# Performance work log

Measured on AMD Instinct MI355X. Metric: run time of the kernel, lower is better.

## Reference

```python
import jax, jax.numpy as jnp
import numpy as np

SQRT_QKV_DIM = 8.0  # sqrt(qkv_dim=64)


def setup_inputs() -> dict:
    key = jax.random.key(0)
    ks = jax.random.split(key, 8)
    B, H, T, M, d, hid = 4, 16, 512, 512, 64, 16
    return {
        "q": jax.random.normal(ks[0], (B, H, T, d), dtype=jnp.float32),
        "k": jax.random.normal(ks[1], (B, H, M, d), dtype=jnp.float32),
        "v": jax.random.normal(ks[2], (B, H, M, d), dtype=jnp.float32),
        "D_TM": jax.random.uniform(ks[3], (B, T, M), dtype=jnp.float32),
        "mix1_weight": jax.random.uniform(ks[4], (H, 2, hid), minval=-0.7071, maxval=0.7071, dtype=jnp.float32),
        "mix1_bias": jax.random.uniform(ks[5], (H, hid), minval=-0.7071, maxval=0.7071, dtype=jnp.float32),
        "mix2_weight": jax.random.uniform(ks[6], (H, hid, 1), minval=-0.25, maxval=0.25, dtype=jnp.float32),
        "mix2_bias": jax.random.uniform(ks[7], (H, 1), minval=-0.25, maxval=0.25, dtype=jnp.float32),
    }


def reference(q, k, v, D_TM, mix1_weight, mix1_bias, mix2_weight, mix2_bias):
    B, H, T, d = q.shape
    Mc = k.shape[2]
    # scaled dot-product score: (B,H,T,M)
    dot_score = jnp.einsum("bhtd,bhmd->bhtm", q, k) / SQRT_QKV_DIM
    # per-head 2->hidden->1 MLP mixing dot score and distance bias.
    # Avoid explicit stack: linear layer over the 2 score channels expands as
    # dot*W1[:,0,:] + D*W1[:,1,:].  ms1: (B,H,T,M,hid)
    w1_dot = mix1_weight[:, 0, :][None, :, None, None, :]   # (1,H,1,1,hid)
    w1_dist = mix1_weight[:, 1, :][None, :, None, None, :]
    ms1 = (dot_score[..., None] * w1_dot
           + D_TM[:, None, :, :, None] * w1_dist
           + mix1_bias[None, :, None, None, :])
    ms1 = jax.nn.relu(ms1)
    # hidden -> 1: mixed_scores (B,H,T,M)
    mixed = jnp.einsum("bhtmc,hc->bhtm", ms1, mix2_weight[:, :, 0])
    mixed = mixed + mix2_bias[:, 0][None, :, None, None]
    weights = jax.nn.softmax(mixed, axis=3)
    out = jnp.einsum("bhtm,bhmd->bhtd", weights, v)   # (B,H,T,d)
    return out.transpose(0, 2, 1, 3).reshape(B, T, H * d)
```

## Files before the change

### kernel.cpp

```cpp
#include <hip/hip_runtime.h>
#include <stdint.h>

typedef __attribute__((ext_vector_type(8))) short short8;
typedef __attribute__((ext_vector_type(4))) float floatx4;

#define MFMA(a, b, c) __builtin_amdgcn_mfma_f32_16x16x32_bf16(a, b, c, 0, 0, 0)

union Frag { uint32_t u[4]; short8 s; };

__device__ __forceinline__ void packsplit(float a, float b, uint32_t& hi, uint32_t& lo) {
    uint32_t ua = __float_as_uint(a), ub = __float_as_uint(b);
    uint32_t ha = ua & 0xFFFF0000u, hb = ub & 0xFFFF0000u;
    float ra = a - __uint_as_float(ha);
    float rb = b - __uint_as_float(hb);
    hi = __builtin_amdgcn_perm(ub, ua, 0x07060302u);
    lo = __builtin_amdgcn_perm(__float_as_uint(rb), __float_as_uint(ra), 0x07060302u);
}

__device__ __forceinline__ float fexp2(float x) {
#if __has_builtin(__builtin_amdgcn_exp2f)
    return __builtin_amdgcn_exp2f(x);
#else
    return exp2f(x);
#endif
}

__device__ __forceinline__ void bar_lds() {
    asm volatile("s_waitcnt lgkmcnt(0)" ::: "memory");
    __builtin_amdgcn_s_barrier();
    __builtin_amdgcn_sched_barrier(0);
}


__attribute__((amdgpu_waves_per_eu(4)))
__global__ __launch_bounds__(512)
void msmha_flash(const float* __restrict__ qg, const float* __restrict__ kg,
                 const float* __restrict__ vg, const float* __restrict__ Dg,
                 const float* __restrict__ m1w, const float* __restrict__ m1b,
                 const float* __restrict__ m2w, const float* __restrict__ m2b,
                 float* __restrict__ outg) {
    __shared__ __align__(16) uint32_t sm[17408];
    __shared__ __align__(16) float4 wlds[16];

    const int tid   = threadIdx.x;
    const int w     = tid >> 6;
    const int group = w >> 2;
    const int gw    = w & 3;
    const int lane  = tid & 63;
    const int col   = lane & 15;
    const int quad  = lane >> 4;
    const int gtid  = tid & 255;

    const int bid = blockIdx.x;
    const int wgT = bid >> 6;
    const int bh  = bid & 63;
    const int h   = bh & 15;
    const int b   = bh >> 4;
    const int t0g = wgT * 64;

    const size_t base = (size_t)bh * 512 * 64;
    const float LOG2E = 1.4426950408889634f;

    if (tid < 16) {
        const float w1d = m1w[h * 32 + tid];
        const float w1s = m1w[h * 32 + 16 + tid];
        const float b1  = m1b[h * 16 + tid];
        const float w2  = m2w[h * 16 + tid];
        wlds[tid] = make_float4(w1d * (0.125f * LOG2E), w1s * LOG2E, b1 * LOG2E, 0.5f * w2);
    }

    const int krow = 16 * gw + (lane >> 2);
    const int kqt  = lane & 3;
    const int ksw  = (krow & 7) << 2;
    const int rsw  = (col & 7) << 2;
    const int dgrp = gtid & 15;
    const int m4   = gtid >> 4;
    const int cpV  = (2 * m4 + 8 * ((dgrp >> 1) & 3)) & 31;
    const int rsel = col >> 3;

    const int gb = group * 8704;
    uint32_t* KH = sm + gb;
    uint32_t* KL = sm + gb + 2048;
    uint32_t* VH = sm + gb + 4096;
    uint32_t* VL = sm + gb + 6400;

    const int moff = group * 256;
    const float* kc = kg + base + (size_t)moff * 64;
    const float* vc = vg + base + (size_t)moff * 64;
    const float* Dc = Dg + ((size_t)b * 512 + t0g + gw * 16 + col) * 512 + moff + quad * 4;

    float sA = 0.f, sB = 0.f, sC = 0.f;
#pragma unroll 1
    for (int c = 0; c < 16; ++c) {
        const float w2 = m2w[h * 16 + c];
        sA = fmaf(w2, m1w[h * 32 + c], sA);
        sB = fmaf(w2, m1w[h * 32 + 16 + c], sB);
        sC = fmaf(w2, m1b[h * 16 + c], sC);
    }
    const float Ac = sA * (0.0625f * LOG2E);
    const float Bc = sB * (0.5f * LOG2E);
    const float Cc = fmaf(0.5f, sC, m2b[h]) * LOG2E;

    Frag qh[2], ql[2];
    {
        const float* qrow = qg + base + (size_t)(t0g + gw * 16 + col) * 64;
#pragma unroll
        for (int ks = 0; ks < 2; ++ks) {
            const float4 f0 = *(const float4*)(qrow + ks * 32 + quad * 8);
            const float4 f1 = *(const float4*)(qrow + ks * 32 + quad * 8 + 4);
            packsplit(f0.x, f0.y, qh[ks].u[0], ql[ks].u[0]);
            packsplit(f0.z, f0.w, qh[ks].u[1], ql[ks].u[1]);
            packsplit(f1.x, f1.y, qh[ks].u[2], ql[ks].u[2]);
            packsplit(f1.z, f1.w, qh[ks].u[3], ql[ks].u[3]);
        }
    }

    float lsum = 0.f;
    floatx4 oacc[4];
#pragma unroll
    for (int dt = 0; dt < 4; ++dt) oacc[dt] = floatx4{0.f, 0.f, 0.f, 0.f};

#pragma unroll 1
    for (int mc = 0; mc < 4; ++mc) {
        float4 kp[4], vp[4], dp[4];
#pragma unroll
        for (int i = 0; i < 4; ++i)
            kp[i] = *(const float4*)(kc + (size_t)(mc * 64 + krow) * 64 + 16 * i + 4 * kqt);
#pragma unroll
        for (int i = 0; i < 4; ++i)
            vp[i] = *(const float4*)(vc + (size_t)(mc * 64 + 4 * m4 + i) * 64 + dgrp * 4);
#pragma unroll
        for (int mt = 0; mt < 4; ++mt)
            dp[mt] = *(const float4*)(Dc + mc * 64 + mt * 16);

#pragma unroll
        for (int i = 0; i < 4; ++i) {
            uint32_t h0, l0, h1, l1;
            packsplit(kp[i].x, kp[i].y, h0, l0);
            packsplit(kp[i].z, kp[i].w, h1, l1);
            const int off = (8 * i + 2 * kqt) ^ ksw;
            *(uint2*)(KH + krow * 32 + off) = make_uint2(h0, h1);
            *(uint2*)(KL + krow * 32 + off) = make_uint2(l0, l1);
        }
        bar_lds();

        floatx4 sc[4];
        __builtin_amdgcn_s_setprio(1);
#pragma unroll
        for (int mt = 0; mt < 4; ++mt) {
            floatx4 acc = {0.f, 0.f, 0.f, 0.f};
#pragma unroll
            for (int ks = 0; ks < 2; ++ks) {
                const int ro = (mt * 16 + col) * 32 + ((16 * ks + 4 * quad) ^ rsw);
                Frag ah, al;
                ah.s = *(const short8*)(KH + ro);
                al.s = *(const short8*)(KL + ro);
                acc = MFMA(ah.s, qh[ks].s, acc);
                acc = MFMA(ah.s, ql[ks].s, acc);
                acc = MFMA(al.s, qh[ks].s, acc);
            }
            sc[mt] = acc;
        }
        __builtin_amdgcn_s_setprio(0);

#pragma unroll
        for (int jj = 0; jj < 4; ++jj) {
            uint32_t h0, l0, h1, l1;
            packsplit(((const float*)&vp[0])[jj], ((const float*)&vp[1])[jj], h0, l0);
            packsplit(((const float*)&vp[2])[jj], ((const float*)&vp[3])[jj], h1, l1);
            const int d = 4 * dgrp + jj;
            *(uint2*)(VH + d * 36 + cpV) = make_uint2(h0, h1);
            *(uint2*)(VL + d * 36 + cpV) = make_uint2(l0, l1);
        }

#pragma unroll
        for (int half = 0; half < 2; ++half) {
            float dvf[8], mix[8];
#pragma unroll
            for (int q2 = 0; q2 < 2; ++q2) {
                const float4 dd = dp[2 * half + q2];
                dvf[q2 * 4 + 0] = dd.x; dvf[q2 * 4 + 1] = dd.y;
                dvf[q2 * 4 + 2] = dd.z; dvf[q2 * 4 + 3] = dd.w;
            }
#pragma unroll
            for (int e = 0; e < 8; ++e) mix[e] = fmaf(dvf[e], Bc, Cc);
#pragma unroll 4
            for (int c = 0; c < 16; ++c) {
                const float4 wv = wlds[c];
#pragma unroll
                for (int e = 0; e < 8; ++e) {
                    const float s = sc[2 * half + (e >> 2)][e & 3];
                    const float hh = fmaf(s, wv.x, fmaf(dvf[e], wv.y, wv.z));
                    mix[e] = fmaf(fabsf(hh), wv.w, mix[e]);
                }
            }
#pragma unroll
            for (int e = 0; e < 8; ++e) {
                const float s = sc[2 * half + (e >> 2)][e & 3];
                const float p = fexp2(fmaf(s, Ac, mix[e]));
                sc[2 * half + (e >> 2)][e & 3] = p;
                lsum += p;
            }
        }

        bar_lds();

        const int prow = (gw * 16 + col) * 32;
#pragma unroll
        for (int mt = 0; mt < 4; ++mt) {
            uint32_t h0, l0, h1, l1;
            packsplit(sc[mt][0], sc[mt][1], h0, l0);
            packsplit(sc[mt][2], sc[mt][3], h1, l1);
            const int off = (mt * 8 + 2 * quad) ^ rsw;
            *(uint2*)(KH + prow + off) = make_uint2(h0, h1);
            *(uint2*)(KL + prow + off) = make_uint2(l0, l1);
        }

        __builtin_amdgcn_s_setprio(1);
#pragma unroll
        for (int ks = 0; ks < 2; ++ks) {
            const int po = prow + ((16 * ks + 4 * quad) ^ rsw);
            Frag pah, pal;
            pah.s = *(const short8*)(KH + po);
            pal.s = *(const short8*)(KL + po);
#pragma unroll
            for (int dt = 0; dt < 4; ++dt) {
                const int cbd = ((16 * ks + 4 * quad) + 8 * ((2 * dt + rsel) & 3)) & 31;
                const int vo = (dt * 16 + col) * 36 + cbd;
                Frag bhv, blv;
                bhv.s = *(const short8*)(VH + vo);
                blv.s = *(const short8*)(VL + vo);
                oacc[dt] = MFMA(pah.s, bhv.s, oacc[dt]);
                oacc[dt] = MFMA(pah.s, blv.s, oacc[dt]);
                oacc[dt] = MFMA(pal.s, bhv.s, oacc[dt]);
            }
        }
        __builtin_amdgcn_s_setprio(0);
    }

    bar_lds();

    lsum += __shfl_xor(lsum, 16, 64);
    lsum += __shfl_xor(lsum, 32, 64);

    float* smf = (float*)sm;
    if (group == 1) {
        if (quad == 0) smf[12864 + gw * 16 + col] = lsum;
        const int t = gw * 16 + quad * 4;
#pragma unroll
        for (int dt = 0; dt < 4; ++dt)
#pragma unroll
            for (int r = 0; r < 4; ++r)
                smf[8704 + (t + r) * 65 + dt * 16 + col] = oacc[dt][r];
    }
    bar_lds();
    if (group == 0) {
        const float l1c = smf[12864 + gw * 16 + col];
        const float rdn = 1.f / (lsum + l1c);
        float rdT[4];
#pragma unroll
        for (int r = 0; r < 4; ++r)
            rdT[r] = __shfl(rdn, quad * 4 + r, 64);
        const int t = gw * 16 + quad * 4;
        const size_t obase = ((size_t)b * 512 + t0g + t) * 1024 + h * 64 + col;
#pragma unroll
        for (int dt = 0; dt < 4; ++dt)
#pragma unroll
            for (int r = 0; r < 4; ++r) {
                const float o1 = smf[8704 + (t + r) * 65 + dt * 16 + col];
                outg[obase + (size_t)r * 1024 + dt * 16] = (oacc[dt][r] + o1) * rdT[r];
            }
    }
}

extern "C" void kernel_launch(void* const* d_in, const int* in_sizes, int n_in,
                              void* d_out, int out_size, void* d_ws, size_t ws_size,
                              hipStream_t stream) {
    const float* q   = (const float*)d_in[0];
    const float* k   = (const float*)d_in[1];
    const float* v   = (const float*)d_in[2];
    const float* dtm = (const float*)d_in[3];
    const float* m1w = (const float*)d_in[4];
    const float* m1b = (const float*)d_in[5];
    const float* m2w = (const float*)d_in[6];
    const float* m2b = (const float*)d_in[7];
    float* out = (float*)d_out;

    dim3 grid(4 * 16 * 8);
    dim3 block(512);
    msmha_flash<<<grid, block, 0, stream>>>(q, k, v, dtm, m1w, m1b, m2w, m2b, out);
}
```

Measured before the change: 123.9 us.

## Pre-pack K/V into bf16 hi/lo split once and vectorize MLP mixing with packed float2

```diff
diff --git a/kernel.cpp b/kernel.cpp
--- a/kernel.cpp
+++ b/kernel.cpp
@@ -3,10 +3,12 @@
 
 typedef __attribute__((ext_vector_type(8))) short short8;
 typedef __attribute__((ext_vector_type(4))) float floatx4;
+typedef __attribute__((ext_vector_type(2))) float float2v;
 
 #define MFMA(a, b, c) __builtin_amdgcn_mfma_f32_16x16x32_bf16(a, b, c, 0, 0, 0)
 
 union Frag { uint32_t u[4]; short8 s; };
+union PF2 { float2v f; uint32_t u[2]; };
 
 __device__ __forceinline__ void packsplit(float a, float b, uint32_t& hi, uint32_t& lo) {
     uint32_t ua = __float_as_uint(a), ub = __float_as_uint(b);
@@ -31,13 +33,53 @@
     __builtin_amdgcn_sched_barrier(0);
 }
 
-
-__attribute__((amdgpu_waves_per_eu(4)))
-__global__ __launch_bounds__(512)
+#define VLO 1048576
+#define KPK_DW 2097152
+#define WS_NEED ((size_t)(KPK_DW + 2 * VLO) * 4)
+
+__global__ __launch_bounds__(256)
+void packkv(const float* __restrict__ kg, const float* __restrict__ vg,
+            uint32_t* __restrict__ kpk, uint32_t* __restrict__ vpk) {
+    const int bid = blockIdx.x, tid = threadIdx.x;
+    if (bid < 2048) {
+        const int g   = bid * 256 + tid;
+        const int row = g >> 4, q = g & 15;
+        const float4 f = *(const float4*)(kg + (size_t)row * 64 + 4 * q);
+        uint32_t h0, l0, h1, l1;
+        packsplit(f.x, f.y, h0, l0);
+        packsplit(f.z, f.w, h1, l1);
+        uint32_t* rb = kpk + (size_t)row * 64;
+        *(uint2*)(rb + 2 * q)      = make_uint2(h0, h1);
+        *(uint2*)(rb + 32 + 2 * q) = make_uint2(l0, l1);
+    } else {
+        const int vb  = bid - 2048;
+        const int bh  = vb >> 4, m2g = vb & 15;
+        const int m2  = m2g * 16 + (tid & 15);
+        const int dg  = tid >> 4;
+        const float* r0 = vg + ((size_t)(bh * 512 + 2 * m2)) * 64 + 4 * dg;
+        const float4 f0 = *(const float4*)(r0);
+        const float4 f1 = *(const float4*)(r0 + 64);
+        const float a0[4] = {f0.x, f0.y, f0.z, f0.w};
+        const float a1[4] = {f1.x, f1.y, f1.z, f1.w};
+#pragma unroll
+        for (int jj = 0; jj < 4; ++jj) {
+            uint32_t hh, ll;
+            packsplit(a0[jj], a1[jj], hh, ll);
+            const size_t o = (size_t)(bh * 64 + 4 * dg + jj) * 256 + m2;
+            vpk[o]       = hh;
+            vpk[VLO + o] = ll;
+        }
+    }
+}
+
+
+template <int PKD>
+__global__ __attribute__((amdgpu_waves_per_eu(4))) __launch_bounds__(512)
 void msmha_flash(const float* __restrict__ qg, const float* __restrict__ kg,
                  const float* __restrict__ vg, const float* __restrict__ Dg,
                  const float* __restrict__ m1w, const float* __restrict__ m1b,
                  const float* __restrict__ m2w, const float* __restrict__ m2b,
+                 const uint32_t* __restrict__ kpk, const uint32_t* __restrict__ vpk,
                  float* __restrict__ outg) {
     __shared__ __align__(16) uint32_t sm[17408];
     __shared__ __align__(16) float4 wlds[16];
@@ -120,86 +162,151 @@
 #pragma unroll
     for (int dt = 0; dt < 4; ++dt) oacc[dt] = floatx4{0.f, 0.f, 0.f, 0.f};
 
+    const float2v Ac2 = {Ac, Ac}, Bc2 = {Bc, Bc}, Cc2 = {Cc, Cc};
+
 #pragma unroll 1
     for (int mc = 0; mc < 4; ++mc) {
-        float4 kp[4], vp[4], dp[4];
-#pragma unroll
-        for (int i = 0; i < 4; ++i)
-            kp[i] = *(const float4*)(kc + (size_t)(mc * 64 + krow) * 64 + 16 * i + 4 * kqt);
-#pragma unroll
-        for (int i = 0; i < 4; ++i)
-            vp[i] = *(const float4*)(vc + (size_t)(mc * 64 + 4 * m4 + i) * 64 + dgrp * 4);
-#pragma unroll
-        for (int mt = 0; mt < 4; ++mt)
-            dp[mt] = *(const float4*)(Dc + mc * 64 + mt * 16);
-
-#pragma unroll
-        for (int i = 0; i < 4; ++i) {
-            uint32_t h0, l0, h1, l1;
-            packsplit(kp[i].x, kp[i].y, h0, l0);
-            packsplit(kp[i].z, kp[i].w, h1, l1);
-            const int off = (8 * i + 2 * kqt) ^ ksw;
-            *(uint2*)(KH + krow * 32 + off) = make_uint2(h0, h1);
-            *(uint2*)(KL + krow * 32 + off) = make_uint2(l0, l1);
-        }
-        bar_lds();
-
+        float4 dp[4];
         floatx4 sc[4];
-        __builtin_amdgcn_s_setprio(1);
-#pragma unroll
-        for (int mt = 0; mt < 4; ++mt) {
-            floatx4 acc = {0.f, 0.f, 0.f, 0.f};
-#pragma unroll
-            for (int ks = 0; ks < 2; ++ks) {
-                const int ro = (mt * 16 + col) * 32 + ((16 * ks + 4 * quad) ^ rsw);
-                Frag ah, al;
-                ah.s = *(const short8*)(KH + ro);
-                al.s = *(const short8*)(KL + ro);
-                acc = MFMA(ah.s, qh[ks].s, acc);
-                acc = MFMA(ah.s, ql[ks].s, acc);
-                acc = MFMA(al.s, qh[ks].s, acc);
-            }
-            sc[mt] = acc;
-        }
-        __builtin_amdgcn_s_setprio(0);
-
-#pragma unroll
-        for (int jj = 0; jj < 4; ++jj) {
-            uint32_t h0, l0, h1, l1;
-            packsplit(((const float*)&vp[0])[jj], ((const float*)&vp[1])[jj], h0, l0);
-            packsplit(((const float*)&vp[2])[jj], ((const float*)&vp[3])[jj], h1, l1);
-            const int d = 4 * dgrp + jj;
-            *(uint2*)(VH + d * 36 + cpV) = make_uint2(h0, h1);
-            *(uint2*)(VL + d * 36 + cpV) = make_uint2(l0, l1);
+
+        if constexpr (PKD) {
+            uint2 khl[4], kll[4], vhl[4], vll[4];
+            const size_t krb = ((size_t)(bh * 512 + moff + mc * 64 + krow)) * 64;
+#pragma unroll
+            for (int i = 0; i < 4; ++i) {
+                khl[i] = *(const uint2*)(kpk + krb + 8 * i + 2 * kqt);
+                kll[i] = *(const uint2*)(kpk + krb + 32 + 8 * i + 2 * kqt);
+            }
+#pragma unroll
+            for (int jj = 0; jj < 4; ++jj) {
+                const size_t vbd = (size_t)(bh * 64 + 4 * dgrp + jj) * 256
+                                 + 128 * group + 32 * mc + 2 * m4;
+                vhl[jj] = *(const uint2*)(vpk + vbd);
+                vll[jj] = *(const uint2*)(vpk + VLO + vbd);
+            }
+#pragma unroll
+            for (int mt = 0; mt < 4; ++mt)
+                dp[mt] = *(const float4*)(Dc + mc * 64 + mt * 16);
+
+#pragma unroll
+            for (int i = 0; i < 4; ++i) {
+                const int off = (8 * i + 2 * kqt) ^ ksw;
+                *(uint2*)(KH + krow * 32 + off) = khl[i];
+                *(uint2*)(KL + krow * 32 + off) = kll[i];
+            }
+            bar_lds();
+
+            __builtin_amdgcn_s_setprio(1);
+#pragma unroll
+            for (int mt = 0; mt < 4; ++mt) {
+                floatx4 acc = {0.f, 0.f, 0.f, 0.f};
+#pragma unroll
+                for (int ks = 0; ks < 2; ++ks) {
+                    const int ro = (mt * 16 + col) * 32 + ((16 * ks + 4 * quad) ^ rsw);
+                    Frag ah, al;
+                    ah.s = *(const short8*)(KH + ro);
+                    al.s = *(const short8*)(KL + ro);
+                    acc = MFMA(ah.s, qh[ks].s, acc);
+                    acc = MFMA(ah.s, ql[ks].s, acc);
+                    acc = MFMA(al.s, qh[ks].s, acc);
+                }
+                sc[mt] = acc;
+            }
+            __builtin_amdgcn_s_setprio(0);
+
+#pragma unroll
+            for (int jj = 0; jj < 4; ++jj) {
+                const int d = 4 * dgrp + jj;
+                *(uint2*)(VH + d * 36 + cpV) = vhl[jj];
+                *(uint2*)(VL + d * 36 + cpV) = vll[jj];
+            }
+        } else {
+            float4 kp[4], vp[4];
+#pragma unroll
+            for (int i = 0; i < 4; ++i)
+                kp[i] = *(const float4*)(kc + (size_t)(mc * 64 + krow) * 64 + 16 * i + 4 * kqt);
+#pragma unroll
+            for (int i = 0; i < 4; ++i)
+                vp[i] = *(const float4*)(vc + (size_t)(mc * 64 + 4 * m4 + i) * 64 + dgrp * 4);
+#pragma unroll
+            for (int mt = 0; mt < 4; ++mt)
+                dp[mt] = *(const float4*)(Dc + mc * 64 + mt * 16);
+
+#pragma unroll
+            for (int i = 0; i < 4; ++i) {
+                uint32_t h0, l0, h1, l1;
+                packsplit(kp[i].x, kp[i].y, h0, l0);
+                packsplit(kp[i].z, kp[i].w, h1, l1);
+                const int off = (8 * i + 2 * kqt) ^ ksw;
+                *(uint2*)(KH + krow * 32 + off) = make_uint2(h0, h1);
+                *(uint2*)(KL + krow * 32 + off) = make_uint2(l0, l1);
+            }
+            bar_lds();
+
+            __builtin_amdgcn_s_setprio(1);
+#pragma unroll
+            for (int mt = 0; mt < 4; ++mt) {
+                floatx4 acc = {0.f, 0.f, 0.f, 0.f};
+#pragma unroll
+                for (int ks = 0; ks < 2; ++ks) {
+                    const int ro = (mt * 16 + col) * 32 + ((16 * ks + 4 * quad) ^ rsw);
+                    Frag ah, al;
+                    ah.s = *(const short8*)(KH + ro);
+                    al.s = *(const short8*)(KL + ro);
+                    acc = MFMA(ah.s, qh[ks].s, acc);
+                    acc = MFMA(ah.s, ql[ks].s, acc);
+                    acc = MFMA(al.s, qh[ks].s, acc);
+                }
+                sc[mt] = acc;
+            }
+            __builtin_amdgcn_s_setprio(0);
+
+#pragma unroll
+            for (int jj = 0; jj < 4; ++jj) {
+                uint32_t h0, l0, h1, l1;
+                packsplit(((const float*)&vp[0])[jj], ((const float*)&vp[1])[jj], h0, l0);
+                packsplit(((const float*)&vp[2])[jj], ((const float*)&vp[3])[jj], h1, l1);
+                const int d = 4 * dgrp + jj;
+                *(uint2*)(VH + d * 36 + cpV) = make_uint2(h0, h1);
+                *(uint2*)(VL + d * 36 + cpV) = make_uint2(l0, l1);
+            }
         }
 
 #pragma unroll
         for (int half = 0; half < 2; ++half) {
-            float dvf[8], mix[8];
-#pragma unroll
-            for (int q2 = 0; q2 < 2; ++q2) {
-                const float4 dd = dp[2 * half + q2];
-                dvf[q2 * 4 + 0] = dd.x; dvf[q2 * 4 + 1] = dd.y;
-                dvf[q2 * 4 + 2] = dd.z; dvf[q2 * 4 + 3] = dd.w;
-            }
-#pragma unroll
-            for (int e = 0; e < 8; ++e) mix[e] = fmaf(dvf[e], Bc, Cc);
+            float2v s2v[4], dv2[4], mx2[4];
+#pragma unroll
+            for (int p = 0; p < 4; ++p) {
+                const int mt = 2 * half + (p >> 1), eo = 2 * (p & 1);
+                s2v[p] = float2v{sc[mt][eo], sc[mt][eo + 1]};
+                const float4 dd = dp[mt];
+                dv2[p] = (p & 1) ? float2v{dd.z, dd.w} : float2v{dd.x, dd.y};
+            }
+#pragma unroll
+            for (int p = 0; p < 4; ++p) mx2[p] = dv2[p] * Bc2 + Cc2;
 #pragma unroll 4
             for (int c = 0; c < 16; ++c) {
                 const float4 wv = wlds[c];
-#pragma unroll
-                for (int e = 0; e < 8; ++e) {
-                    const float s = sc[2 * half + (e >> 2)][e & 3];
-                    const float hh = fmaf(s, wv.x, fmaf(dvf[e], wv.y, wv.z));
-                    mix[e] = fmaf(fabsf(hh), wv.w, mix[e]);
+                const float2v wx2 = {wv.x, wv.x}, wy2 = {wv.y, wv.y};
+                const float2v wz2 = {wv.z, wv.z}, ww2 = {wv.w, wv.w};
+#pragma unroll
+                for (int p = 0; p < 4; ++p) {
+                    PF2 a;
+                    a.f = s2v[p] * wx2 + (dv2[p] * wy2 + wz2);
+                    a.u[0] &= 0x7fffffffu;
+                    a.u[1] &= 0x7fffffffu;
+                    mx2[p] = a.f * ww2 + mx2[p];
                 }
             }
 #pragma unroll
-            for (int e = 0; e < 8; ++e) {
-                const float s = sc[2 * half + (e >> 2)][e & 3];
-                const float p = fexp2(fmaf(s, Ac, mix[e]));
-                sc[2 * half + (e >> 2)][e & 3] = p;
-                lsum += p;
+            for (int p = 0; p < 4; ++p) {
+                const float2v sco = s2v[p] * Ac2 + mx2[p];
+                const float px = fexp2(sco.x), py = fexp2(sco.y);
+                const int mt = 2 * half + (p >> 1), eo = 2 * (p & 1);
+                sc[mt][eo]     = px;
+                sc[mt][eo + 1] = py;
+                lsum += px;
+                lsum += py;
             }
         }
 
@@ -288,5 +395,15 @@
 
     dim3 grid(4 * 16 * 8);
     dim3 block(512);
-    msmha_flash<<<grid, block, 0, stream>>>(q, k, v, dtm, m1w, m1b, m2w, m2b, out);
-}
+
+    if (d_ws != nullptr && ws_size >= WS_NEED) {
+        uint32_t* kpk = (uint32_t*)d_ws;
+        uint32_t* vpk = kpk + KPK_DW;
+        packkv<<<dim3(3072), dim3(256), 0, stream>>>(k, v, kpk, vpk);
+        msmha_flash<1><<<grid, block, 0, stream>>>(q, k, v, dtm, m1w, m1b, m2w, m2b,
+                                                   kpk, vpk, out);
+    } else {
+        msmha_flash<0><<<grid, block, 0, stream>>>(q, k, v, dtm, m1w, m1b, m2w, m2b,
+                                                   nullptr, nullptr, out);
+    }
+}
```

Measured after the change: 136.1 us. 1.1x slower.
